# Optimization experiments

Measured on AMD Instinct MI355X. Metric: run time of the kernel, lower is better.

The kernel has to match this reference:

```python
import jax, jax.numpy as jnp
import numpy as np

EPS = 1e-5

@jax.custom_vjp
def sign_ste(x):
    # BinActivation / weight binarization: sign(x) in {-1,+1}
    return jnp.where(x >= 0, 1.0, -1.0).astype(x.dtype)

def _sign_fwd(x):
    return sign_ste(x), x

def _sign_bwd(x, g):
    # straight-through estimator with hardtanh clipping: pass grad where |x| <= 1
    return (g * (jnp.abs(x) <= 1.0).astype(g.dtype),)

sign_ste.defvjp(_sign_fwd, _sign_bwd)

def setup_inputs() -> dict:
    key = jax.random.key(0)
    k1, k2 = jax.random.split(key)
    x = jax.random.normal(k1, (32, 256, 56, 56), dtype=jnp.float32)
    W = jax.random.normal(k2, (256, 256, 3, 3), dtype=jnp.float32) * 0.1
    gamma = jnp.ones((256,), dtype=jnp.float32)
    beta = jnp.zeros((256,), dtype=jnp.float32)
    return {"x": x, "W": W, "gamma": gamma, "beta": beta}

def reference(x, W, gamma, beta):
    # binarize activation and weights to {-1,+1}
    xb = sign_ste(x)
    wb = sign_ste(W)
    # conv: NCHW x OIHW -> NCHW, stride 1, padding 1, dilation 1, no bias
    y = jax.lax.conv_general_dilated(
        xb, wb,
        window_strides=(1, 1),
        padding=[(1, 1), (1, 1)],
        rhs_dilation=(1, 1),
        dimension_numbers=("NCHW", "OIHW", "NCHW"),
    )
    # BatchNorm2d in training mode: batch statistics over (N,H,W), affine
    mean = jnp.mean(y, axis=(0, 2, 3), keepdims=True)          # [1,C,1,1]
    var = jnp.mean((y - mean) ** 2, axis=(0, 2, 3), keepdims=True)
    y = (y - mean) * jax.lax.rsqrt(var + EPS)
    y = y * gamma[None, :, None, None] + beta[None, :, None, None]
    # Hardtanh(-1, 1)
    return jnp.clip(y, -1.0, 1.0)
```

## Files before the change

kernel.cpp:

```cpp
#include <hip/hip_runtime.h>
#include <stdint.h>
#include <math.h>

#define N_IMG 32
#define C_IN  256
#define HW    56
#define P_PIX (HW*HW)
#define P4    (P_PIX/4)
#define OC    256
#define WPC   8
#define NPIX  (N_IMG*P_PIX)
#define NTOT  ((double)N_IMG*(double)P_PIX)
#define WSTRIDE 80

__global__ __launch_bounds__(256) void pack_x_kernel(const float* __restrict__ x,
                                                     uint32_t* __restrict__ px) {
    int idx  = blockIdx.x * 256 + threadIdx.x;
    int word = idx / NPIX;
    int r    = idx - word * NPIX;
    int n    = r / P_PIX;
    int p    = r - n * P_PIX;
    const float* xp = x + ((size_t)(n * C_IN + word * 32)) * P_PIX + p;
    uint32_t bits = 0;
#pragma unroll
    for (int k = 0; k < 32; ++k) {
        float v = xp[(size_t)k * P_PIX];
        bits |= (v >= 0.0f) ? (1u << k) : 0u;
    }
    px[((size_t)(n * P_PIX + p)) * WPC + word] = bits;
}

__global__ void pack_w_kernel(const float* __restrict__ Wt,
                              uint32_t* __restrict__ wp,
                              int* __restrict__ corr,
                              long long* __restrict__ sums,
                              long long* __restrict__ sumsq) {
    __shared__ int lpop[72];
    __shared__ int ltap[9];
    int o = blockIdx.x;
    int t = threadIdx.x;
    if (t == 0) { sums[o] = 0; sumsq[o] = 0; }
    if (t < 72) {
        int tap = t >> 3;
        int word = t & 7;
        const float* wpr = Wt + ((size_t)(o * C_IN + word * 32)) * 9 + tap;
        uint32_t bits = 0;
#pragma unroll
        for (int k = 0; k < 32; ++k) {
            float v = wpr[(size_t)k * 9];
            bits |= (v >= 0.0f) ? (1u << k) : 0u;
        }
        wp[o * WSTRIDE + t] = bits;
        lpop[t] = __popc(bits);
    }
    __syncthreads();
    if (t < 9) {
        int s = 0;
#pragma unroll
        for (int w = 0; w < 8; ++w) s += lpop[t * 8 + w];
        ltap[t] = s;
    }
    __syncthreads();
    if (t < 9) {
        int vc = t / 3, hc = t % 3;
        int c = 0;
        for (int dy = -1; dy <= 1; ++dy)
            for (int dx = -1; dx <= 1; ++dx) {
                bool inv = (dy == -1 && vc == 1) || (dy == 1 && vc == 2) ||
                           (dx == -1 && hc == 1) || (dx == 1 && hc == 2);
                if (inv) {
                    int tap = (dy + 1) * 3 + (dx + 1);
                    c += 256 - 2 * ltap[tap];
                }
            }
        corr[o * 9 + t] = c;
    }
}

template <typename YT>
__global__ __launch_bounds__(128) void bconv_kernel(const uint32_t* __restrict__ px,
                                                    const uint32_t* __restrict__ wp,
                                                    const int* __restrict__ corr,
                                                    YT* __restrict__ yout,
                                                    long long* __restrict__ sums,
                                                    long long* __restrict__ sumsq) {
    __shared__ int ls[64];
    __shared__ int lq[64];
    int blk  = blockIdx.x;
    int pc   = blk >> 2;
    int osec = blk & 3;
    int gi   = pc * 128 + threadIdx.x;
    int n = gi / P_PIX;
    int p = gi - n * P_PIX;
    int h = p / HW;
    int w = p - h * HW;

    if (threadIdx.x < 64) { ls[threadIdx.x] = 0; lq[threadIdx.x] = 0; }

    uint32_t xr[72];
#pragma unroll
    for (int i = 0; i < 9; ++i) {
        int dy = i / 3 - 1, dx = i % 3 - 1;
        int hh = h + dy, ww = w + dx;
        bool valid = (hh >= 0) && (hh < HW) && (ww >= 0) && (ww < HW);
        const uint4* src = (const uint4*)(px + ((size_t)(n * P_PIX + hh * HW + ww)) * WPC);
        uint4 a = valid ? src[0] : make_uint4(0u, 0u, 0u, 0u);
        uint4 b = valid ? src[1] : make_uint4(0u, 0u, 0u, 0u);
        xr[i * 8 + 0] = a.x; xr[i * 8 + 1] = a.y; xr[i * 8 + 2] = a.z; xr[i * 8 + 3] = a.w;
        xr[i * 8 + 4] = b.x; xr[i * 8 + 5] = b.y; xr[i * 8 + 6] = b.z; xr[i * 8 + 7] = b.w;
    }

    int vc = (h == 0) ? 1 : ((h == HW - 1) ? 2 : 0);
    int hc = (w == 0) ? 1 : ((w == HW - 1) ? 2 : 0);
    const int* cptr = corr + vc * 3 + hc;
    __syncthreads();

    int o0 = osec * 64;
    YT* yp = yout + ((size_t)(n * OC + o0)) * P_PIX + p;
    for (int oo = 0; oo < 64; ++oo) {
        int o = o0 + oo;
        const uint4* wq = (const uint4*)(wp + o * WSTRIDE);
        int acc = 0;
#pragma unroll
        for (int j = 0; j < 18; ++j) {
            uint4 wv = wq[j];
            acc += __popc(xr[4 * j + 0] ^ wv.x);
            acc += __popc(xr[4 * j + 1] ^ wv.y);
            acc += __popc(xr[4 * j + 2] ^ wv.z);
            acc += __popc(xr[4 * j + 3] ^ wv.w);
        }
        int v = 2304 - 2 * acc - cptr[o * 9];
        *yp = (YT)v;
        yp += P_PIX;
        int s = v, q = v * v;
#pragma unroll
        for (int off = 32; off > 0; off >>= 1) {
            s += __shfl_xor(s, off, 64);
            q += __shfl_xor(q, off, 64);
        }
        if ((threadIdx.x & 63) == 0) {
            atomicAdd(&ls[oo], s);
            atomicAdd(&lq[oo], q);
        }
    }
    __syncthreads();
    if (threadIdx.x < 64) {
        atomicAdd((unsigned long long*)&sums[o0 + threadIdx.x],
                  (unsigned long long)(long long)ls[threadIdx.x]);
        atomicAdd((unsigned long long*)&sumsq[o0 + threadIdx.x],
                  (unsigned long long)(long long)lq[threadIdx.x]);
    }
}

template <typename YT>
__global__ __launch_bounds__(256) void apply_kernel(const YT* __restrict__ y,
                                                    float* __restrict__ out,
                                                    const long long* __restrict__ sums,
                                                    const long long* __restrict__ sumsq,
                                                    const float* __restrict__ gamma,
                                                    const float* __restrict__ beta) {
    int o = blockIdx.x;
    double invN = 1.0 / NTOT;
    double mean = (double)sums[o] * invN;
    double var  = (double)sumsq[o] * invN - mean * mean;
    double sc   = (double)gamma[o] / sqrt(var + 1e-5);
    float s = (float)sc;
    float b = (float)((double)beta[o] - mean * sc);
    for (int idx = threadIdx.x; idx < N_IMG * P4; idx += 256) {
        int n  = idx / P4;
        int p4 = idx - n * P4;
        size_t base = ((size_t)(n * OC + o)) * P_PIX + 4 * p4;
        float4 v;
        const YT* src = y + base;
        v.x = (float)src[0]; v.y = (float)src[1]; v.z = (float)src[2]; v.w = (float)src[3];
        v.x = fminf(fmaxf(fmaf(v.x, s, b), -1.0f), 1.0f);
        v.y = fminf(fmaxf(fmaf(v.y, s, b), -1.0f), 1.0f);
        v.z = fminf(fmaxf(fmaf(v.z, s, b), -1.0f), 1.0f);
        v.w = fminf(fmaxf(fmaf(v.w, s, b), -1.0f), 1.0f);
        *(float4*)(out + base) = v;
    }
}

extern "C" void kernel_launch(void* const* d_in, const int* in_sizes, int n_in,
                              void* d_out, int out_size, void* d_ws, size_t ws_size,
                              hipStream_t stream) {
    const float* x     = (const float*)d_in[0];
    const float* Wt    = (const float*)d_in[1];
    const float* gamma = (const float*)d_in[2];
    const float* beta  = (const float*)d_in[3];
    float* out = (float*)d_out;
    char* ws = (char*)d_ws;

    uint32_t*  px    = (uint32_t*) (ws);
    uint32_t*  wp    = (uint32_t*) (ws + 3211264);
    int*       corr  = (int*)      (ws + 3293184);
    long long* sums  = (long long*)(ws + 3302400);
    long long* sumsq = (long long*)(ws + 3304448);
    short*     y16   = (short*)    (ws + 3306496);
    const size_t WS_NEED_I16 = 3306496ull + 51380224ull;

    hipLaunchKernelGGL(pack_x_kernel, dim3(8 * NPIX / 256), dim3(256), 0, stream, x, px);
    hipLaunchKernelGGL(pack_w_kernel, dim3(OC), dim3(128), 0, stream, Wt, wp, corr, sums, sumsq);
    if (ws_size >= WS_NEED_I16) {
        hipLaunchKernelGGL(bconv_kernel<short>, dim3((NPIX / 128) * 4), dim3(128), 0, stream,
                           px, wp, corr, y16, sums, sumsq);
        hipLaunchKernelGGL(apply_kernel<short>, dim3(OC), dim3(256), 0, stream,
                           y16, out, sums, sumsq, gamma, beta);
    } else {
        hipLaunchKernelGGL(bconv_kernel<float>, dim3((NPIX / 128) * 4), dim3(128), 0, stream,
                           px, wp, corr, out, sums, sumsq);
        hipLaunchKernelGGL(apply_kernel<float>, dim3(OC), dim3(256), 0, stream,
                           out, out, sums, sumsq, gamma, beta);
    }
}
```

Before: 403.5 us.

## Restructure binary conv: weights in registers, row-per-block, NHWC int16 output with transposing apply

The binary conv kernel now assigns one output channel per thread with its 72 packed weight words held in registers, and each block processes one image row. Activations are read as wave-uniform broadcast loads, and a zero row handles padding. The intermediate is stored pixel-major with channels contiguous, and the apply kernel transposes it through LDS to write NCHW floats. pack_x is vectorized to process four pixels per thread. The aim is to replace per-output weight reloads and wave-level reductions with register reuse, at the cost of strided 2-byte stores per thread and an extra transpose.

```diff
diff --git a/kernel.cpp b/kernel.cpp
--- a/kernel.cpp
+++ b/kernel.cpp
@@ -6,28 +6,39 @@
 #define C_IN  256
 #define HW    56
 #define P_PIX (HW*HW)
-#define P4    (P_PIX/4)
 #define OC    256
 #define WPC   8
 #define NPIX  (N_IMG*P_PIX)
 #define NTOT  ((double)N_IMG*(double)P_PIX)
-#define WSTRIDE 80
 
 __global__ __launch_bounds__(256) void pack_x_kernel(const float* __restrict__ x,
-                                                     uint32_t* __restrict__ px) {
-    int idx  = blockIdx.x * 256 + threadIdx.x;
-    int word = idx / NPIX;
-    int r    = idx - word * NPIX;
-    int n    = r / P_PIX;
-    int p    = r - n * P_PIX;
-    const float* xp = x + ((size_t)(n * C_IN + word * 32)) * P_PIX + p;
-    uint32_t bits = 0;
+                                                     uint32_t* __restrict__ px,
+                                                     uint32_t* __restrict__ zero_row) {
+    int blk = blockIdx.x;
+    if (blk == 784) {
+        if (threadIdx.x < 112) ((uint4*)zero_row)[threadIdx.x] = make_uint4(0u,0u,0u,0u);
+        return;
+    }
+    int idx  = blk * 256 + threadIdx.x;
+    int word = idx / 25088;
+    int r    = idx - word * 25088;
+    int n    = r / 784;
+    int p4   = r - n * 784;
+    const float* xp = x + ((size_t)(n * C_IN + word * 32)) * P_PIX + p4 * 4;
+    uint32_t b0 = 0, b1 = 0, b2 = 0, b3 = 0;
 #pragma unroll
     for (int k = 0; k < 32; ++k) {
-        float v = xp[(size_t)k * P_PIX];
-        bits |= (v >= 0.0f) ? (1u << k) : 0u;
-    }
-    px[((size_t)(n * P_PIX + p)) * WPC + word] = bits;
+        float4 v = *(const float4*)(xp + (size_t)k * P_PIX);
+        b0 |= (v.x >= 0.0f) ? (1u << k) : 0u;
+        b1 |= (v.y >= 0.0f) ? (1u << k) : 0u;
+        b2 |= (v.z >= 0.0f) ? (1u << k) : 0u;
+        b3 |= (v.w >= 0.0f) ? (1u << k) : 0u;
+    }
+    uint32_t* dst = px + ((size_t)(n * P_PIX + p4 * 4)) * WPC + word;
+    dst[0]  = b0;
+    dst[8]  = b1;
+    dst[16] = b2;
+    dst[24] = b3;
 }
 
 __global__ void pack_w_kernel(const float* __restrict__ Wt,
@@ -50,7 +61,7 @@
             float v = wpr[(size_t)k * 9];
             bits |= (v >= 0.0f) ? (1u << k) : 0u;
         }
-        wp[o * WSTRIDE + t] = bits;
+        wp[o * 72 + t] = bits;
         lpop[t] = __popc(bits);
     }
     __syncthreads();
@@ -77,107 +88,148 @@
     }
 }
 
-template <typename YT>
-__global__ __launch_bounds__(128) void bconv_kernel(const uint32_t* __restrict__ px,
-                                                    const uint32_t* __restrict__ wp,
-                                                    const int* __restrict__ corr,
-                                                    YT* __restrict__ yout,
-                                                    long long* __restrict__ sums,
-                                                    long long* __restrict__ sumsq) {
-    __shared__ int ls[64];
-    __shared__ int lq[64];
-    int blk  = blockIdx.x;
-    int pc   = blk >> 2;
-    int osec = blk & 3;
-    int gi   = pc * 128 + threadIdx.x;
-    int n = gi / P_PIX;
-    int p = gi - n * P_PIX;
-    int h = p / HW;
-    int w = p - h * HW;
-
-    if (threadIdx.x < 64) { ls[threadIdx.x] = 0; lq[threadIdx.x] = 0; }
-
-    uint32_t xr[72];
-#pragma unroll
-    for (int i = 0; i < 9; ++i) {
-        int dy = i / 3 - 1, dx = i % 3 - 1;
-        int hh = h + dy, ww = w + dx;
-        bool valid = (hh >= 0) && (hh < HW) && (ww >= 0) && (ww < HW);
-        const uint4* src = (const uint4*)(px + ((size_t)(n * P_PIX + hh * HW + ww)) * WPC);
-        uint4 a = valid ? src[0] : make_uint4(0u, 0u, 0u, 0u);
-        uint4 b = valid ? src[1] : make_uint4(0u, 0u, 0u, 0u);
-        xr[i * 8 + 0] = a.x; xr[i * 8 + 1] = a.y; xr[i * 8 + 2] = a.z; xr[i * 8 + 3] = a.w;
-        xr[i * 8 + 4] = b.x; xr[i * 8 + 5] = b.y; xr[i * 8 + 6] = b.z; xr[i * 8 + 7] = b.w;
-    }
-
-    int vc = (h == 0) ? 1 : ((h == HW - 1) ? 2 : 0);
-    int hc = (w == 0) ? 1 : ((w == HW - 1) ? 2 : 0);
-    const int* cptr = corr + vc * 3 + hc;
-    __syncthreads();
-
-    int o0 = osec * 64;
-    YT* yp = yout + ((size_t)(n * OC + o0)) * P_PIX + p;
-    for (int oo = 0; oo < 64; ++oo) {
-        int o = o0 + oo;
-        const uint4* wq = (const uint4*)(wp + o * WSTRIDE);
-        int acc = 0;
-#pragma unroll
-        for (int j = 0; j < 18; ++j) {
-            uint4 wv = wq[j];
-            acc += __popc(xr[4 * j + 0] ^ wv.x);
-            acc += __popc(xr[4 * j + 1] ^ wv.y);
-            acc += __popc(xr[4 * j + 2] ^ wv.z);
-            acc += __popc(xr[4 * j + 3] ^ wv.w);
-        }
-        int v = 2304 - 2 * acc - cptr[o * 9];
-        *yp = (YT)v;
-        yp += P_PIX;
-        int s = v, q = v * v;
-#pragma unroll
-        for (int off = 32; off > 0; off >>= 1) {
-            s += __shfl_xor(s, off, 64);
-            q += __shfl_xor(q, off, 64);
-        }
-        if ((threadIdx.x & 63) == 0) {
-            atomicAdd(&ls[oo], s);
-            atomicAdd(&lq[oo], q);
-        }
-    }
-    __syncthreads();
-    if (threadIdx.x < 64) {
-        atomicAdd((unsigned long long*)&sums[o0 + threadIdx.x],
-                  (unsigned long long)(long long)ls[threadIdx.x]);
-        atomicAdd((unsigned long long*)&sumsq[o0 + threadIdx.x],
-                  (unsigned long long)(long long)lq[threadIdx.x]);
-    }
-}
-
-template <typename YT>
-__global__ __launch_bounds__(256) void apply_kernel(const YT* __restrict__ y,
+__device__ __forceinline__ int dot72(const uint32_t* p0, const uint32_t* p1, const uint32_t* p2,
+                                     const uint32_t* p3, const uint32_t* p4, const uint32_t* p5,
+                                     const uint32_t* p6, const uint32_t* p7, const uint32_t* p8,
+                                     const uint32_t* wreg) {
+    const uint32_t* ps[9] = {p0, p1, p2, p3, p4, p5, p6, p7, p8};
+    int a0 = 0, a1 = 0, a2 = 0, a3 = 0;
+#pragma unroll
+    for (int t = 0; t < 9; ++t) {
+        uint4 a = ((const uint4*)ps[t])[0];
+        uint4 b = ((const uint4*)ps[t])[1];
+        a0 += __popc(a.x ^ wreg[t * 8 + 0]);
+        a1 += __popc(a.y ^ wreg[t * 8 + 1]);
+        a2 += __popc(a.z ^ wreg[t * 8 + 2]);
+        a3 += __popc(a.w ^ wreg[t * 8 + 3]);
+        a0 += __popc(b.x ^ wreg[t * 8 + 4]);
+        a1 += __popc(b.y ^ wreg[t * 8 + 5]);
+        a2 += __popc(b.z ^ wreg[t * 8 + 6]);
+        a3 += __popc(b.w ^ wreg[t * 8 + 7]);
+    }
+    return a0 + a1 + a2 + a3;
+}
+
+__global__ __launch_bounds__(256, 2) void bconv_kernel(const uint32_t* __restrict__ px,
+                                                       const uint32_t* __restrict__ wp,
+                                                       const int* __restrict__ corr,
+                                                       const uint32_t* __restrict__ zero_row,
+                                                       short* __restrict__ y16t,
+                                                       long long* __restrict__ sums,
+                                                       long long* __restrict__ sumsq) {
+    int o   = threadIdx.x;
+    int blk = blockIdx.x;
+    int n = blk / HW, h = blk - n * HW;
+
+    uint32_t wreg[72];
+    const uint4* wq = (const uint4*)(wp + o * 72);
+#pragma unroll
+    for (int j = 0; j < 18; ++j) {
+        uint4 v = wq[j];
+        wreg[4 * j + 0] = v.x; wreg[4 * j + 1] = v.y;
+        wreg[4 * j + 2] = v.z; wreg[4 * j + 3] = v.w;
+    }
+    int vc  = (h == 0) ? 1 : ((h == HW - 1) ? 2 : 0);
+    int crM = corr[o * 9 + vc * 3 + 0];
+    int crL = corr[o * 9 + vc * 3 + 1];
+    int crR = corr[o * 9 + vc * 3 + 2];
+
+    const uint32_t* rowb = px + (size_t)(n * P_PIX) * WPC;
+    const uint32_t* rp0 = (h > 0)      ? rowb + (h - 1) * HW * WPC : zero_row;
+    const uint32_t* rp1 = rowb + h * HW * WPC;
+    const uint32_t* rp2 = (h < HW - 1) ? rowb + (h + 1) * HW * WPC : zero_row;
+
+    short* yp = y16t + ((size_t)(n * P_PIX + h * HW)) * OC + o;
+    int s = 0, q = 0;
+
+    {
+        int acc = dot72(zero_row, rp0, rp0 + 8,
+                        zero_row, rp1, rp1 + 8,
+                        zero_row, rp2, rp2 + 8, wreg);
+        int v = 2304 - 2 * acc - crL;
+        yp[0] = (short)v;
+        s += v; q += __mul24(v, v);
+    }
+    const uint32_t* c0 = rp0;
+    const uint32_t* c1 = rp1;
+    const uint32_t* c2 = rp2;
+    for (int w = 1; w <= HW - 2; ++w) {
+        c0 += 8; c1 += 8; c2 += 8;
+        int acc = dot72(c0 - 8, c0, c0 + 8,
+                        c1 - 8, c1, c1 + 8,
+                        c2 - 8, c2, c2 + 8, wreg);
+        int v = 2304 - 2 * acc - crM;
+        yp[(size_t)w * OC] = (short)v;
+        s += v; q += __mul24(v, v);
+    }
+    {
+        const uint32_t* e0 = rp0 + (HW - 1) * 8;
+        const uint32_t* e1 = rp1 + (HW - 1) * 8;
+        const uint32_t* e2 = rp2 + (HW - 1) * 8;
+        int acc = dot72(e0 - 8, e0, zero_row,
+                        e1 - 8, e1, zero_row,
+                        e2 - 8, e2, zero_row, wreg);
+        int v = 2304 - 2 * acc - crR;
+        yp[(size_t)(HW - 1) * OC] = (short)v;
+        s += v; q += __mul24(v, v);
+    }
+    atomicAdd((unsigned long long*)&sums[o],  (unsigned long long)(long long)s);
+    atomicAdd((unsigned long long*)&sumsq[o], (unsigned long long)(long long)q);
+}
+
+__global__ __launch_bounds__(256) void apply_kernel(const short* __restrict__ y16t,
                                                     float* __restrict__ out,
                                                     const long long* __restrict__ sums,
                                                     const long long* __restrict__ sumsq,
                                                     const float* __restrict__ gamma,
                                                     const float* __restrict__ beta) {
-    int o = blockIdx.x;
-    double invN = 1.0 / NTOT;
-    double mean = (double)sums[o] * invN;
-    double var  = (double)sumsq[o] * invN - mean * mean;
-    double sc   = (double)gamma[o] / sqrt(var + 1e-5);
-    float s = (float)sc;
-    float b = (float)((double)beta[o] - mean * sc);
-    for (int idx = threadIdx.x; idx < N_IMG * P4; idx += 256) {
-        int n  = idx / P4;
-        int p4 = idx - n * P4;
-        size_t base = ((size_t)(n * OC + o)) * P_PIX + 4 * p4;
-        float4 v;
-        const YT* src = y + base;
-        v.x = (float)src[0]; v.y = (float)src[1]; v.z = (float)src[2]; v.w = (float)src[3];
-        v.x = fminf(fmaxf(fmaf(v.x, s, b), -1.0f), 1.0f);
-        v.y = fminf(fmaxf(fmaf(v.y, s, b), -1.0f), 1.0f);
-        v.z = fminf(fmaxf(fmaf(v.z, s, b), -1.0f), 1.0f);
-        v.w = fminf(fmaxf(fmaf(v.w, s, b), -1.0f), 1.0f);
-        *(float4*)(out + base) = v;
+    __shared__ float sbf[512];
+    __shared__ uint32_t tile[64 * 129];
+    int t = threadIdx.x;
+    {
+        int o = t;
+        double invN = 1.0 / NTOT;
+        double mean = (double)sums[o] * invN;
+        double var  = (double)sumsq[o] * invN - mean * mean;
+        double sc   = (double)gamma[o] / sqrt(var + 1e-5);
+        sbf[o]       = (float)sc;
+        sbf[256 + o] = (float)((double)beta[o] - mean * sc);
+    }
+    int blk = blockIdx.x;
+    int n   = blk / 49;
+    int pl0 = (blk - n * 49) * 64;
+    size_t P0 = (size_t)n * P_PIX + pl0;
+#pragma unroll
+    for (int r = 0; r < 8; ++r) {
+        int f8  = r * 256 + t;
+        int pxl = f8 >> 5;
+        int c8  = f8 & 31;
+        uint4 v = *(const uint4*)(y16t + (P0 + pxl) * OC + c8 * 8);
+        uint32_t* d = &tile[pxl * 129 + c8 * 4];
+        d[0] = v.x; d[1] = v.y; d[2] = v.z; d[3] = v.w;
+    }
+    __syncthreads();
+    int lane = t & 63, wv = t >> 6;
+    int lp = lane & 15, lc = lane >> 4;
+    int px0 = lp * 4;
+#pragma unroll
+    for (int i = 0; i < 16; ++i) {
+        int ch = i * 16 + wv * 4 + lc;
+        float sc = sbf[ch], bi = sbf[256 + ch];
+        int sh = (ch & 1) << 4;
+        int ci = ch >> 1;
+        float4 ov;
+        {
+            int v0 = (int)(short)(tile[(px0 + 0) * 129 + ci] >> sh);
+            int v1 = (int)(short)(tile[(px0 + 1) * 129 + ci] >> sh);
+            int v2 = (int)(short)(tile[(px0 + 2) * 129 + ci] >> sh);
+            int v3 = (int)(short)(tile[(px0 + 3) * 129 + ci] >> sh);
+            ov.x = fminf(fmaxf(fmaf((float)v0, sc, bi), -1.0f), 1.0f);
+            ov.y = fminf(fmaxf(fmaf((float)v1, sc, bi), -1.0f), 1.0f);
+            ov.z = fminf(fmaxf(fmaf((float)v2, sc, bi), -1.0f), 1.0f);
+            ov.w = fminf(fmaxf(fmaf((float)v3, sc, bi), -1.0f), 1.0f);
+        }
+        *(float4*)(out + ((size_t)(n * OC + ch)) * P_PIX + pl0 + px0) = ov;
     }
 }
 
@@ -191,25 +243,18 @@
     float* out = (float*)d_out;
     char* ws = (char*)d_ws;
 
-    uint32_t*  px    = (uint32_t*) (ws);
-    uint32_t*  wp    = (uint32_t*) (ws + 3211264);
-    int*       corr  = (int*)      (ws + 3293184);
-    long long* sums  = (long long*)(ws + 3302400);
-    long long* sumsq = (long long*)(ws + 3304448);
-    short*     y16   = (short*)    (ws + 3306496);
-    const size_t WS_NEED_I16 = 3306496ull + 51380224ull;
-
-    hipLaunchKernelGGL(pack_x_kernel, dim3(8 * NPIX / 256), dim3(256), 0, stream, x, px);
-    hipLaunchKernelGGL(pack_w_kernel, dim3(OC), dim3(128), 0, stream, Wt, wp, corr, sums, sumsq);
-    if (ws_size >= WS_NEED_I16) {
-        hipLaunchKernelGGL(bconv_kernel<short>, dim3((NPIX / 128) * 4), dim3(128), 0, stream,
-                           px, wp, corr, y16, sums, sumsq);
-        hipLaunchKernelGGL(apply_kernel<short>, dim3(OC), dim3(256), 0, stream,
-                           y16, out, sums, sumsq, gamma, beta);
-    } else {
-        hipLaunchKernelGGL(bconv_kernel<float>, dim3((NPIX / 128) * 4), dim3(128), 0, stream,
-                           px, wp, corr, out, sums, sumsq);
-        hipLaunchKernelGGL(apply_kernel<float>, dim3(OC), dim3(256), 0, stream,
-                           out, out, sums, sumsq, gamma, beta);
-    }
-}
+    uint32_t*  px       = (uint32_t*) (ws);
+    uint32_t*  wp       = (uint32_t*) (ws + 3211264);
+    int*       corr     = (int*)      (ws + 3284992);
+    long long* sums     = (long long*)(ws + 3294208);
+    long long* sumsq    = (long long*)(ws + 3296256);
+    uint32_t*  zero_row = (uint32_t*) (ws + 3298304);
+    short*     y16t     = (short*)    (ws + 3300352);
+
+    hipLaunchKernelGGL(pack_x_kernel, dim3(785),  dim3(256), 0, stream, x, px, zero_row);
+    hipLaunchKernelGGL(pack_w_kernel, dim3(OC),   dim3(128), 0, stream, Wt, wp, corr, sums, sumsq);
+    hipLaunchKernelGGL(bconv_kernel,  dim3(1792), dim3(256), 0, stream, px, wp, corr, zero_row,
+                       y16t, sums, sumsq);
+    hipLaunchKernelGGL(apply_kernel,  dim3(1568), dim3(256), 0, stream, y16t, out,
+                       sums, sumsq, gamma, beta);
+}
```

New measurement: 470.8 us. 1.17x slower.
